# Kernel optimization log

Measured on AMD Instinct MI355X. Metric: run time of the kernel, lower is better.

Reference implementation:

```python
import jax, jax.numpy as jnp
import numpy as np

D_MODEL = 1024
NHEAD = 16
DFF = 4096
MAXD = 32


def _ln(x, g, b, eps=1e-5):
    mu = jnp.mean(x, axis=-1, keepdims=True)
    var = jnp.mean(jnp.square(x - mu), axis=-1, keepdims=True)
    return (x - mu) * jax.lax.rsqrt(var + eps) * g + b


def setup_inputs() -> dict:
    key = jax.random.key(0)
    ks = jax.random.split(key, 16)
    D, F, H = D_MODEL, DFF, NHEAD
    s = 1.0 / np.sqrt(D)
    inp = {
        "src": jax.random.normal(ks[0], (2, 2048, D), dtype=jnp.float32),
        "Wq": jax.random.normal(ks[1], (D, D), dtype=jnp.float32) * s,
        "Wk": jax.random.normal(ks[2], (D, D), dtype=jnp.float32) * s,
        "Wv": jax.random.normal(ks[3], (D, D), dtype=jnp.float32) * s,
        "bq": jnp.zeros((D,), jnp.float32),
        "bk": jnp.zeros((D,), jnp.float32),
        "bv": jnp.zeros((D,), jnp.float32),
        "Wo": jax.random.normal(ks[4], (D, D), dtype=jnp.float32) * s,
        "bo": jnp.zeros((D,), jnp.float32),
        "rpe_table": jax.random.normal(ks[5], (2 * MAXD + 1, H), dtype=jnp.float32) * 0.02,
        "W1": jax.random.normal(ks[6], (D, F), dtype=jnp.float32) * s,
        "b1": jnp.zeros((F,), jnp.float32),
        "W2": jax.random.normal(ks[7], (F, D), dtype=jnp.float32) * (1.0 / np.sqrt(F)),
        "b2": jnp.zeros((D,), jnp.float32),
        "ln1_g": jnp.ones((D,), jnp.float32),
        "ln1_b": jnp.zeros((D,), jnp.float32),
        "ln2_g": jnp.ones((D,), jnp.float32),
        "ln2_b": jnp.zeros((D,), jnp.float32),
    }
    return inp


def reference(src, Wq, Wk, Wv, bq, bk, bv, Wo, bo, rpe_table, W1, b1, W2, b2,
              ln1_g, ln1_b, ln2_g, ln2_b):
    B, L, D = src.shape
    H = NHEAD
    Dh = D // H
    scale = 1.0 / jnp.sqrt(jnp.asarray(Dh, src.dtype))

    # relative position bias: [L, L, H] -> [H, L, L]
    pos = jnp.arange(L)
    rel = jnp.clip(pos[None, :] - pos[:, None], -MAXD, MAXD) + MAXD  # [L, L]
    bias = jnp.transpose(rpe_table[rel], (2, 0, 1))  # [H, L, L]

    q = (src @ Wq + bq).reshape(B, L, H, Dh)
    k = (src @ Wk + bk).reshape(B, L, H, Dh)
    v = (src @ Wv + bv).reshape(B, L, H, Dh)

    scores = jnp.einsum("blhd,bmhd->bhlm", q, k) * scale + bias[None]
    attn = jax.nn.softmax(scores, axis=-1)
    ctx = jnp.einsum("bhlm,bmhd->blhd", attn, v).reshape(B, L, D)
    attn_out = ctx @ Wo + bo

    x = _ln(src + attn_out, ln1_g, ln1_b)
    ff = jax.nn.relu(x @ W1 + b1) @ W2 + b2
    return _ln(x + ff, ln2_g, ln2_b)
```

## Files before the change

kernel.cpp:

```cpp
#include <hip/hip_runtime.h>
#include <hip/hip_bf16.h>

#define D_MODEL 1024
#define NHEAD 16
#define DH 64
#define DFF 4096
#define MAXD 32
#define L_ 2048
#define NROW 4096

typedef __attribute__((ext_vector_type(4))) float floatx4;
typedef __attribute__((ext_vector_type(8))) __bf16 bf16x8;
typedef __attribute__((ext_vector_type(4))) unsigned short ushort4v;

static __device__ inline unsigned short f2bf(float f) {
    __hip_bfloat16 h = __float2bfloat16(f);
    return __builtin_bit_cast(unsigned short, h);
}

static __device__ inline floatx4 mfma16(bf16x8 a, bf16x8 b, floatx4 c) {
    return __builtin_amdgcn_mfma_f32_16x16x32_bf16(a, b, c, 0, 0, 0);
}

static __device__ inline void gload_lds16(const unsigned short* g, unsigned short* l) {
    __builtin_amdgcn_global_load_lds((const __attribute__((address_space(1))) unsigned int*)g,
                                     (__attribute__((address_space(3))) unsigned int*)l,
                                     16, 0, 0);
}

__global__ __launch_bounds__(256) void cast_bf16_kernel(const float* __restrict__ in,
                                                        unsigned short* __restrict__ out, int n4) {
    int i = blockIdx.x * 256 + threadIdx.x;
    if (i < n4) {
        floatx4 v = *(const floatx4*)&in[(size_t)i * 4];
        ushort4v o;
        o.x = f2bf(v[0]); o.y = f2bf(v[1]); o.z = f2bf(v[2]); o.w = f2bf(v[3]);
        *(ushort4v*)&out[(size_t)i * 4] = o;
    }
}

__global__ __launch_bounds__(256) void transpose_cast_kernel(const float* __restrict__ W,
                                                             unsigned short* __restrict__ WT,
                                                             int K, int N) {
    __shared__ float tile[32][33];
    int k0 = blockIdx.y * 32, n0 = blockIdx.x * 32;
    for (int i = threadIdx.x; i < 1024; i += 256) {
        int r = i >> 5, c = i & 31;
        tile[r][c] = W[(size_t)(k0 + r) * N + n0 + c];
    }
    __syncthreads();
    for (int i = threadIdx.x; i < 1024; i += 256) {
        int r = i >> 5, c = i & 31;
        WT[(size_t)(n0 + r) * K + k0 + c] = f2bf(tile[c][r]);
    }
}

__global__ __launch_bounds__(256) void pack_bias_kernel(const float* __restrict__ bq,
                                                        const float* __restrict__ bk,
                                                        const float* __restrict__ bv,
                                                        float* __restrict__ out) {
    int i = blockIdx.x * 256 + threadIdx.x;
    if (i < 3072) out[i] = (i < 1024) ? bq[i] : ((i < 2048) ? bk[i - 1024] : bv[i - 2048]);
}

template <int NF, bool OUTBF16, bool RELU>
__global__ __launch_bounds__(256) void gemm_kernel(const unsigned short* __restrict__ A,
                                                   const unsigned short* __restrict__ BT,
                                                   const float* __restrict__ bias,
                                                   void* __restrict__ Cout,
                                                   int M, int N, int K) {
    constexpr int BN = NF * 32;
    __shared__ unsigned short Asm[128][32];
    __shared__ unsigned short Bsm[BN][32];
    int t = threadIdx.x;
    int lane = t & 63, w = t >> 6;
    int wm = w >> 1, wn = w & 1;
    int lr = lane & 15, hg = lane >> 4;
    int m0 = blockIdx.y * 128, n0 = blockIdx.x * BN;

    floatx4 acc[4][NF];
#pragma unroll
    for (int i = 0; i < 4; i++)
#pragma unroll
        for (int j = 0; j < NF; j++) acc[i][j] = (floatx4)0.0f;

    int r0 = t >> 2, c0 = (t & 3) * 8;

    for (int k0 = 0; k0 < K; k0 += 32) {
        __syncthreads();
        gload_lds16(&A[(size_t)(m0 + r0) * K + k0 + c0], &Asm[r0][c0]);
        gload_lds16(&A[(size_t)(m0 + r0 + 64) * K + k0 + c0], &Asm[r0 + 64][c0]);
        gload_lds16(&BT[(size_t)(n0 + r0) * K + k0 + c0], &Bsm[r0][c0]);
        if (NF == 4)
            gload_lds16(&BT[(size_t)(n0 + r0 + 64) * K + k0 + c0], &Bsm[r0 + 64][c0]);
        __syncthreads();
        bf16x8 af[4], bfg[NF];
#pragma unroll
        for (int mf = 0; mf < 4; mf++) af[mf] = *(const bf16x8*)&Asm[wm * 64 + mf * 16 + lr][hg * 8];
#pragma unroll
        for (int nf = 0; nf < NF; nf++)
            bfg[nf] = *(const bf16x8*)&Bsm[wn * NF * 16 + nf * 16 + lr][hg * 8];
#pragma unroll
        for (int mf = 0; mf < 4; mf++)
#pragma unroll
            for (int nf = 0; nf < NF; nf++) acc[mf][nf] = mfma16(af[mf], bfg[nf], acc[mf][nf]);
    }

#pragma unroll
    for (int mf = 0; mf < 4; mf++)
#pragma unroll
        for (int nf = 0; nf < NF; nf++) {
            int col = n0 + wn * NF * 16 + nf * 16 + lr;
            float bv = bias[col];
#pragma unroll
            for (int r = 0; r < 4; r++) {
                int row = m0 + wm * 64 + mf * 16 + hg * 4 + r;
                float v = acc[mf][nf][r] + bv;
                if (RELU) v = v > 0.f ? v : 0.f;
                if (OUTBF16)
                    ((unsigned short*)Cout)[(size_t)row * N + col] = f2bf(v);
                else
                    ((float*)Cout)[(size_t)row * N + col] = v;
            }
        }
}

__global__ __launch_bounds__(512, 4) void attn_kernel(const unsigned short* __restrict__ qkv,
                                                      const float* __restrict__ rpe,
                                                      unsigned short* __restrict__ ctx) {
    __shared__ unsigned short Kb0[64 * 64];
    __shared__ unsigned short Kb1[64 * 64];
    __shared__ unsigned short Vt[64 * 64];
    __shared__ unsigned short Ps[8][16 * 64];
    __shared__ float rpl[65];

    const int t = threadIdx.x;
    const int lane = t & 63, w = t >> 6;
    const int lr = lane & 15, hg = lane >> 4;
    const int lrs = (lr & 7) ^ (lr >> 3);

    const int blk = blockIdx.x;
    const int qb = blk & 15;
    const int h = (blk >> 4) & 15;
    const int b = blk >> 8;
    const int q0 = qb * 128;
    const int hcol = h * 64;
    const size_t rowbase = (size_t)b * L_ * 3072;

    const int kr = t >> 3, kch = t & 7;
    const int kswz = (kch ^ (kr & 7) ^ (kr >> 3)) & 7;
    unsigned short* kdst0 = &Kb0[kr * 64 + kch * 8];
    unsigned short* kdst1 = &Kb1[kr * 64 + kch * 8];

    if (t < 65) rpl[t] = rpe[t * NHEAD + h];

    const int qi = q0 + w * 16 + lr;
    bf16x8 qf0 = *(const bf16x8*)&qkv[rowbase + (size_t)qi * 3072 + hcol + hg * 8];
    bf16x8 qf1 = *(const bf16x8*)&qkv[rowbase + (size_t)qi * 3072 + hcol + 32 + hg * 8];

    gload_lds16(&qkv[rowbase + (size_t)kr * 3072 + 1024 + hcol + kswz * 8], kdst0);
    __syncthreads();

    float rpl0 = rpl[0], rpl64 = rpl[64];
    floatx4 o[4];
#pragma unroll
    for (int df = 0; df < 4; df++) o[df] = (floatx4)0.f;
    float mst = -1e30f, lst = 0.f;
    const float scale = 0.125f;
    unsigned short* PsW = &Ps[w][0];

#define ATT_STEP(KT, KcP, KnP, MORE)                                                               \
    {                                                                                              \
        const int key0 = (KT) * 64;                                                                \
        int4 tv = *(const int4*)&qkv[rowbase + (size_t)(key0 + kr) * 3072 + 2048 + hcol + kch * 8];\
        if (MORE)                                                                                  \
            gload_lds16(&qkv[rowbase + (size_t)(key0 + 64 + kr) * 3072 + 1024 + hcol + kswz * 8],  \
                        KnP);                                                                      \
        floatx4 st[4];                                                                             \
        _Pragma("unroll")                                                                          \
        for (int kf = 0; kf < 4; kf++) {                                                           \
            int sw = lrs ^ (kf * 2);                                                               \
            bf16x8 a0 = *(const bf16x8*)&(KcP)[(kf * 16 + lr) * 64 + ((hg ^ sw) << 3)];            \
            bf16x8 a1 = *(const bf16x8*)&(KcP)[(kf * 16 + lr) * 64 + (((4 + hg) ^ sw) << 3)];      \
            st[kf] = mfma16(a1, qf1, mfma16(a0, qf0, (floatx4)0.f));                               \
        }                                                                                          \
        bool rightC = (key0 > q0 + 159);                                                           \
        bool leftC = (key0 + 95 < q0);                                                             \
        float cbv = rightC ? rpl64 : rpl0;                                                         \
        float sv[16];                                                                              \
        float mx = -1e30f;                                                                         \
        if (leftC || rightC) {                                                                     \
            _Pragma("unroll")                                                                      \
            for (int kf = 0; kf < 4; kf++)                                                         \
                _Pragma("unroll")                                                                  \
                for (int r = 0; r < 4; r++) {                                                      \
                    float v = st[kf][r] * scale + cbv;                                             \
                    sv[kf * 4 + r] = v;                                                            \
                    mx = fmaxf(mx, v);                                                             \
                }                                                                                  \
        } else {                                                                                   \
            _Pragma("unroll")                                                                      \
            for (int kf = 0; kf < 4; kf++)                                                         \
                _Pragma("unroll")                                                                  \
                for (int r = 0; r < 4; r++) {                                                      \
                    int rel = key0 + kf * 16 + hg * 4 + r - qi;                                    \
                    rel = rel < -MAXD ? -MAXD : (rel > MAXD ? MAXD : rel);                         \
                    float v = st[kf][r] * scale + rpl[rel + MAXD];                                 \
                    sv[kf * 4 + r] = v;                                                            \
                    mx = fmaxf(mx, v);                                                             \
                }                                                                                  \
        }                                                                                          \
        mx = fmaxf(mx, __shfl_xor(mx, 16, 64));                                                    \
        mx = fmaxf(mx, __shfl_xor(mx, 32, 64));                                                    \
        float newm = fmaxf(mst, mx);                                                               \
        float corr = __expf(mst - newm);                                                           \
        mst = newm;                                                                                \
        float ps = 0.f;                                                                            \
        unsigned int pk[8];                                                                        \
        _Pragma("unroll")                                                                          \
        for (int kf = 0; kf < 4; kf++)                                                             \
            _Pragma("unroll")                                                                      \
            for (int j = 0; j < 2; j++) {                                                          \
                float p0 = __expf(sv[kf * 4 + 2 * j] - newm);                                      \
                float p1 = __expf(sv[kf * 4 + 2 * j + 1] - newm);                                  \
                ps += p0 + p1;                                                                     \
                pk[kf * 2 + j] = (unsigned int)f2bf(p0) | ((unsigned int)f2bf(p1) << 16);          \
            }                                                                                      \
        lst = lst * corr + ps;                                                                     \
        _Pragma("unroll")                                                                          \
        for (int df = 0; df < 4; df++) o[df] *= corr;                                              \
        _Pragma("unroll")                                                                          \
        for (int kf = 0; kf < 4; kf++)                                                             \
            _Pragma("unroll")                                                                      \
            for (int j = 0; j < 2; j++) {                                                          \
                int ch = ((kf * 2 + (hg >> 1)) ^ lrs) & 7;                                         \
                *(unsigned int*)&PsW[lr * 64 + (ch << 3) + (hg & 1) * 4 + 2 * j] = pk[kf * 2 + j]; \
            }                                                                                      \
        _Pragma("unroll")                                                                          \
        for (int e = 0; e < 8; e++) {                                                              \
            int d = kch * 8 + e;                                                                   \
            int ch = ((kr >> 3) ^ e ^ kch) & 7;                                                    \
            unsigned short val = (unsigned short)(((const unsigned int*)&tv)[e >> 1] >>            \
                                                  ((e & 1) * 16));                                 \
            Vt[d * 64 + (ch << 3) + (kr & 7)] = val;                                               \
        }                                                                                          \
        __syncthreads();                                                                           \
        bf16x8 pb0 = *(const bf16x8*)&PsW[lr * 64 + ((hg ^ lrs) << 3)];                            \
        bf16x8 pb1 = *(const bf16x8*)&PsW[lr * 64 + (((4 + hg) ^ lrs) << 3)];                      \
        _Pragma("unroll")                                                                          \
        for (int df = 0; df < 4; df++) {                                                           \
            int sw = lrs ^ (df * 2);                                                               \
            bf16x8 v0 = *(const bf16x8*)&Vt[(df * 16 + lr) * 64 + ((hg ^ sw) << 3)];               \
            bf16x8 v1 = *(const bf16x8*)&Vt[(df * 16 + lr) * 64 + (((4 + hg) ^ sw) << 3)];         \
            o[df] = mfma16(v1, pb1, mfma16(v0, pb0, o[df]));                                       \
        }                                                                                          \
        __syncthreads();                                                                           \
    }

    for (int kt = 0; kt < L_ / 64; kt += 2) {
        ATT_STEP(kt, Kb0, kdst1, true);
        ATT_STEP(kt + 1, Kb1, kdst0, (kt + 2 < L_ / 64));
    }
#undef ATT_STEP

    float rs = lst;
    rs += __shfl_xor(rs, 16, 64);
    rs += __shfl_xor(rs, 32, 64);
    float inv = 1.f / rs;
    size_t obase = (size_t)(b * L_ + qi) * 1024 + hcol;
#pragma unroll
    for (int df = 0; df < 4; df++)
#pragma unroll
        for (int r = 0; r < 4; r++)
            ctx[obase + df * 16 + hg * 4 + r] = f2bf(o[df][r] * inv);
}

template <bool WBF>
__global__ __launch_bounds__(256) void resln_kernel(const float* __restrict__ ra,
                                                    const float* __restrict__ rb,
                                                    const float* __restrict__ g,
                                                    const float* __restrict__ be,
                                                    float* __restrict__ outf,
                                                    unsigned short* __restrict__ outb) {
    __shared__ float red[4];
    __shared__ float red2[4];
    int row = blockIdx.x;
    int t = threadIdx.x;
    int w = t >> 6, lane = t & 63;
    size_t base = (size_t)row * 1024 + t * 4;
    floatx4 a = *(const floatx4*)&ra[base];
    floatx4 b = *(const floatx4*)&rb[base];
    floatx4 y = a + b;
    float s = y[0] + y[1] + y[2] + y[3];
#pragma unroll
    for (int d = 1; d < 64; d <<= 1) s += __shfl_xor(s, d, 64);
    if (lane == 0) red[w] = s;
    __syncthreads();
    float mu = (red[0] + red[1] + red[2] + red[3]) * (1.f / 1024.f);
    floatx4 d4 = y - mu;
    float sq = d4[0] * d4[0] + d4[1] * d4[1] + d4[2] * d4[2] + d4[3] * d4[3];
#pragma unroll
    for (int d = 1; d < 64; d <<= 1) sq += __shfl_xor(sq, d, 64);
    if (lane == 0) red2[w] = sq;
    __syncthreads();
    float var = (red2[0] + red2[1] + red2[2] + red2[3]) * (1.f / 1024.f);
    float rstd = rsqrtf(var + 1e-5f);
    floatx4 gg = *(const floatx4*)&g[t * 4];
    floatx4 bb = *(const floatx4*)&be[t * 4];
    floatx4 outv;
#pragma unroll
    for (int i = 0; i < 4; i++) outv[i] = d4[i] * rstd * gg[i] + bb[i];
    *(floatx4*)&outf[base] = outv;
    if (WBF) {
        ushort4v ov;
        ov.x = f2bf(outv[0]); ov.y = f2bf(outv[1]); ov.z = f2bf(outv[2]); ov.w = f2bf(outv[3]);
        *(ushort4v*)&outb[base] = ov;
    }
}

extern "C" void kernel_launch(void* const* d_in, const int* in_sizes, int n_in,
                              void* d_out, int out_size, void* d_ws, size_t ws_size,
                              hipStream_t stream) {
    const float* src = (const float*)d_in[0];
    const float* Wq = (const float*)d_in[1];
    const float* Wk = (const float*)d_in[2];
    const float* Wv = (const float*)d_in[3];
    const float* bq = (const float*)d_in[4];
    const float* bk = (const float*)d_in[5];
    const float* bv = (const float*)d_in[6];
    const float* Wo = (const float*)d_in[7];
    const float* bo = (const float*)d_in[8];
    const float* rpe = (const float*)d_in[9];
    const float* W1 = (const float*)d_in[10];
    const float* b1 = (const float*)d_in[11];
    const float* W2 = (const float*)d_in[12];
    const float* b2 = (const float*)d_in[13];
    const float* ln1g = (const float*)d_in[14];
    const float* ln1b = (const float*)d_in[15];
    const float* ln2g = (const float*)d_in[16];
    const float* ln2b = (const float*)d_in[17];
    float* out = (float*)d_out;
    char* ws = (char*)d_ws;

    const size_t o_srcb = 0;
    const size_t o_wtqkv = o_srcb + 8388608;
    const size_t o_wto = o_wtqkv + 6291456;
    const size_t o_wt1 = o_wto + 2097152;
    const size_t o_wt2 = o_wt1 + 8388608;
    const size_t o_bqkv = o_wt2 + 8388608;
    const size_t o_qkv = o_bqkv + 12288;
    const size_t o_ctxb = o_qkv + 25165824;
    const size_t o_x = o_ctxb + 8388608;
    const size_t o_hb = o_x + 16777216;

    unsigned short* srcb = (unsigned short*)(ws + o_srcb);
    unsigned short* wtqkv = (unsigned short*)(ws + o_wtqkv);
    unsigned short* wto = (unsigned short*)(ws + o_wto);
    unsigned short* wt1 = (unsigned short*)(ws + o_wt1);
    unsigned short* wt2 = (unsigned short*)(ws + o_wt2);
    float* bqkv = (float*)(ws + o_bqkv);
    unsigned short* qkvb = (unsigned short*)(ws + o_qkv);
    unsigned short* ctxb = (unsigned short*)(ws + o_ctxb);
    float* x = (float*)(ws + o_x);
    unsigned short* hb = (unsigned short*)(ws + o_hb);
    float* attnout = (float*)(ws + o_qkv);
    float* ff = (float*)(ws + o_qkv);
    unsigned short* xb = (unsigned short*)(ws + o_srcb);

    cast_bf16_kernel<<<4096, 256, 0, stream>>>(src, srcb, 1048576);
    transpose_cast_kernel<<<dim3(32, 32), 256, 0, stream>>>(Wq, wtqkv, 1024, 1024);
    transpose_cast_kernel<<<dim3(32, 32), 256, 0, stream>>>(Wk, wtqkv + 1024 * 1024, 1024, 1024);
    transpose_cast_kernel<<<dim3(32, 32), 256, 0, stream>>>(Wv, wtqkv + 2 * 1024 * 1024, 1024, 1024);
    transpose_cast_kernel<<<dim3(32, 32), 256, 0, stream>>>(Wo, wto, 1024, 1024);
    transpose_cast_kernel<<<dim3(128, 32), 256, 0, stream>>>(W1, wt1, 1024, 4096);
    transpose_cast_kernel<<<dim3(32, 128), 256, 0, stream>>>(W2, wt2, 4096, 1024);
    pack_bias_kernel<<<12, 256, 0, stream>>>(bq, bk, bv, bqkv);

    gemm_kernel<4, true, false><<<dim3(24, 32), 256, 0, stream>>>(srcb, wtqkv, bqkv, qkvb, NROW, 3072, 1024);
    attn_kernel<<<512, 512, 0, stream>>>(qkvb, rpe, ctxb);
    gemm_kernel<2, false, false><<<dim3(16, 32), 256, 0, stream>>>(ctxb, wto, bo, attnout, NROW, 1024, 1024);
    resln_kernel<true><<<4096, 256, 0, stream>>>(src, attnout, ln1g, ln1b, x, xb);
    gemm_kernel<4, true, true><<<dim3(32, 32), 256, 0, stream>>>(xb, wt1, b1, hb, NROW, 4096, 1024);
    gemm_kernel<2, false, false><<<dim3(16, 32), 256, 0, stream>>>(hb, wt2, b2, ff, NROW, 1024, 4096);
    resln_kernel<false><<<4096, 256, 0, stream>>>(x, ff, ln2g, ln2b, out, nullptr);
}
```

Measured before the change: 346.3 us.

## Double GEMM K-tile to 64 with XOR-swizzled LDS and remap attention block order

```diff
diff --git a/kernel.cpp b/kernel.cpp
--- a/kernel.cpp
+++ b/kernel.cpp
@@ -70,8 +70,8 @@
                                                    void* __restrict__ Cout,
                                                    int M, int N, int K) {
     constexpr int BN = NF * 32;
-    __shared__ unsigned short Asm[128][32];
-    __shared__ unsigned short Bsm[BN][32];
+    __shared__ unsigned short Asm[128][64];
+    __shared__ unsigned short Bsm[BN][64];
     int t = threadIdx.x;
     int lane = t & 63, w = t >> 6;
     int wm = w >> 1, wn = w & 1;
@@ -84,26 +84,40 @@
 #pragma unroll
         for (int j = 0; j < NF; j++) acc[i][j] = (floatx4)0.0f;
 
-    int r0 = t >> 2, c0 = (t & 3) * 8;
-
-    for (int k0 = 0; k0 < K; k0 += 32) {
+    const int lr7 = lr & 7;
+
+    for (int k0 = 0; k0 < K; k0 += 64) {
         __syncthreads();
-        gload_lds16(&A[(size_t)(m0 + r0) * K + k0 + c0], &Asm[r0][c0]);
-        gload_lds16(&A[(size_t)(m0 + r0 + 64) * K + k0 + c0], &Asm[r0 + 64][c0]);
-        gload_lds16(&BT[(size_t)(n0 + r0) * K + k0 + c0], &Bsm[r0][c0]);
-        if (NF == 4)
-            gload_lds16(&BT[(size_t)(n0 + r0 + 64) * K + k0 + c0], &Bsm[r0 + 64][c0]);
+#pragma unroll
+        for (int i = 0; i < 4; i++) {
+            int c = t + i * 256;
+            int r = c >> 3, ch = c & 7;
+            int chs = ch ^ (r & 7);
+            gload_lds16(&A[(size_t)(m0 + r) * K + k0 + chs * 8], &Asm[r][ch * 8]);
+        }
+#pragma unroll
+        for (int i = 0; i < BN / 32; i++) {
+            int c = t + i * 256;
+            int r = c >> 3, ch = c & 7;
+            int chs = ch ^ (r & 7);
+            gload_lds16(&BT[(size_t)(n0 + r) * K + k0 + chs * 8], &Bsm[r][ch * 8]);
+        }
         __syncthreads();
-        bf16x8 af[4], bfg[NF];
-#pragma unroll
-        for (int mf = 0; mf < 4; mf++) af[mf] = *(const bf16x8*)&Asm[wm * 64 + mf * 16 + lr][hg * 8];
-#pragma unroll
-        for (int nf = 0; nf < NF; nf++)
-            bfg[nf] = *(const bf16x8*)&Bsm[wn * NF * 16 + nf * 16 + lr][hg * 8];
-#pragma unroll
-        for (int mf = 0; mf < 4; mf++)
-#pragma unroll
-            for (int nf = 0; nf < NF; nf++) acc[mf][nf] = mfma16(af[mf], bfg[nf], acc[mf][nf]);
+#pragma unroll
+        for (int kc = 0; kc < 2; kc++) {
+            int ch = (kc * 4 + hg) ^ lr7;
+            bf16x8 af[4], bfg[NF];
+#pragma unroll
+            for (int mf = 0; mf < 4; mf++)
+                af[mf] = *(const bf16x8*)&Asm[wm * 64 + mf * 16 + lr][ch * 8];
+#pragma unroll
+            for (int nf = 0; nf < NF; nf++)
+                bfg[nf] = *(const bf16x8*)&Bsm[wn * NF * 16 + nf * 16 + lr][ch * 8];
+#pragma unroll
+            for (int mf = 0; mf < 4; mf++)
+#pragma unroll
+                for (int nf = 0; nf < NF; nf++) acc[mf][nf] = mfma16(af[mf], bfg[nf], acc[mf][nf]);
+        }
     }
 
 #pragma unroll
@@ -139,7 +153,8 @@
     const int lr = lane & 15, hg = lane >> 4;
     const int lrs = (lr & 7) ^ (lr >> 3);
 
-    const int blk = blockIdx.x;
+    const int g = blockIdx.x;
+    const int blk = (g & 7) * 64 + (g >> 3);
     const int qb = blk & 15;
     const int h = (blk >> 4) & 15;
     const int b = blk >> 8;
```

After: 310.0 us. 1.12x faster.
